# Kernel optimization log

Hardware: AMD Instinct MI355X
Metric: run time of the kernel (lower is better)

Reference implementation:

```python
import jax, jax.numpy as jnp
import numpy as np

B, T, D, S, K = 4, 4096, 1024, 2048, 4
LN_EPS = 1e-5


def setup_inputs() -> dict:
    key = jax.random.key(0)
    ks = jax.random.split(key, 9)
    scale = 0.02
    return {
        "x": jax.random.normal(ks[0], (B, T, D), jnp.float32),
        "W_in": jax.random.normal(ks[1], (D, 2 * S), jnp.float32) * scale,
        "b_in": jnp.zeros((2 * S,), jnp.float32),
        "conv_w": jax.random.normal(ks[2], (S, 1, K), jnp.float32) * scale,  # depthwise [out_ch, in_ch/groups=1, K]
        "conv_b": jnp.zeros((S,), jnp.float32),
        "W_out": jax.random.normal(ks[3], (S, D), jnp.float32) * scale,
        "b_out": jnp.zeros((D,), jnp.float32),
        "gamma": jnp.ones((D,), jnp.float32),
        "beta": jnp.zeros((D,), jnp.float32),
    }


def reference(x, W_in, b_in, conv_w, conv_b, W_out, b_out, gamma, beta):
    # x: [B, T, D]
    residual = x
    proj = x @ W_in + b_in                      # [B, T, 2S]
    mixed, gate = jnp.split(proj, 2, axis=-1)   # each [B, T, S]
    mixed = mixed * jax.nn.sigmoid(gate)
    h = jnp.transpose(mixed, (0, 2, 1))         # [B, S, T]
    k = conv_w.shape[-1]
    # torch pads both sides by K-1 then slices [:T] -> equivalent to causal left-pad K-1
    y = jax.lax.conv_general_dilated(
        h, conv_w,
        window_strides=(1,),
        padding=[(k - 1, 0)],
        dimension_numbers=("NCH", "OIH", "NCH"),
        feature_group_count=conv_w.shape[0],
    ) + conv_b[None, :, None]                   # [B, S, T]
    y = jnp.transpose(y, (0, 2, 1))             # [B, T, S]
    y = y @ W_out + b_out                       # [B, T, D]
    z = residual + y                            # dropout p=0.0 -> identity
    mu = jnp.mean(z, axis=-1, keepdims=True)
    var = jnp.var(z, axis=-1, keepdims=True)
    zn = (z - mu) * jax.lax.rsqrt(var + LN_EPS)
    return zn * gamma + beta
```

## Files before the change

### kernel.cpp

```cpp
#include <hip/hip_runtime.h>
#include <hip/hip_bf16.h>


#define Bdim 4
#define Tdim 4096
#define Ddim 1024
#define Sdim 2048
#define Mdim (Bdim * Tdim)
#define LN_EPS 1e-5f

typedef __bf16 bf16;
typedef __bf16 bf16x8 __attribute__((ext_vector_type(8)));
typedef float f32x4 __attribute__((ext_vector_type(4)));

#define BAR() __builtin_amdgcn_s_barrier()
#define SCHED() __builtin_amdgcn_sched_barrier(0)
#define LGKM0() asm volatile("s_waitcnt lgkmcnt(0)" ::: "memory")
#define VMCNT4() asm volatile("s_waitcnt vmcnt(4)" ::: "memory")
#define VMCNT0() asm volatile("s_waitcnt vmcnt(0)" ::: "memory")

__device__ __forceinline__ void gload_lds16(const bf16* g, bf16* l) {
  __builtin_amdgcn_global_load_lds((const __attribute__((address_space(1))) void*)g,
                                   (__attribute__((address_space(3))) void*)l,
                                   16, 0, 0);
}

__device__ __forceinline__ f32x4 zero4() {
  f32x4 z; z[0] = 0.f; z[1] = 0.f; z[2] = 0.f; z[3] = 0.f; return z;
}

__global__ __launch_bounds__(256) void k_cast_x(const float* __restrict__ x,
                                                bf16* __restrict__ xb) {
  int gid = blockIdx.x * 256 + threadIdx.x;
  const float4* p = (const float4*)x + (size_t)gid * 2;
  float4 a = p[0], b = p[1];
  bf16x8 o;
  o[0] = (bf16)a.x; o[1] = (bf16)a.y; o[2] = (bf16)a.z; o[3] = (bf16)a.w;
  o[4] = (bf16)b.x; o[5] = (bf16)b.y; o[6] = (bf16)b.z; o[7] = (bf16)b.w;
  ((bf16x8*)xb)[gid] = o;
}

__global__ __launch_bounds__(256) void k_transpose_cast(const float* __restrict__ in,
                                                        bf16* __restrict__ out,
                                                        int R, int C, int permmode) {
  __shared__ float tile[32][33];
  int tx = threadIdx.x & 31;
  int ty = threadIdx.x >> 5;
  int r0 = blockIdx.y * 32;
  int c0 = blockIdx.x * 32;
#pragma unroll
  for (int i = 0; i < 4; ++i)
    tile[ty + i * 8][tx] = in[(size_t)(r0 + ty + i * 8) * C + c0 + tx];
  __syncthreads();
#pragma unroll
  for (int i = 0; i < 4; ++i) {
    int oc = c0 + ty + i * 8;
    int pr = oc;
    if (permmode) {
      pr = (oc < 2048) ? ((oc >> 4) * 32 + (oc & 15))
                       : (((oc - 2048) >> 4) * 32 + 16 + (oc & 15));
    }
    out[(size_t)pr * R + r0 + tx] = (bf16)tile[tx][ty + i * 8];
  }
}

template<int KTOT, int NTN, int EPI>
__global__ __launch_bounds__(512, 1)
void k_gemm256(const bf16* __restrict__ Ag, const bf16* __restrict__ Bg,
               const float* __restrict__ bias, const float* __restrict__ xres,
               bf16* __restrict__ outb, float* __restrict__ outf) {
  __shared__ __attribute__((aligned(16))) char lds[131072];

  const int tid = threadIdx.x;
  const int w = tid >> 6, lane = tid & 63;
  const int lr = lane & 15, lk = lane >> 4;
  const int wr = w >> 2, wc = w & 3;

  const int nwg = gridDim.x;
  const int bid = blockIdx.x;
  const int wg = (bid & 7) * (nwg >> 3) + (bid >> 3);
  const int m0 = (wg / NTN) * 256;
  const int n0 = (wg % NTN) * 256;

  const int dlin = lane * 16;
  const int lsw = dlin ^ (((dlin >> 7) & 7) << 4);
  const int rw = lsw >> 7;
  const int cw = (lsw & 127) >> 1;

  const int xmask = (lr & 7) << 4;
  const int arow = lr * 128;
  const int brow = ((wc & 1) * 64 + lr) * 128;
  const char* ldsA = lds + wr * 16384;
  const char* ldsB = lds + 32768 + (wc >> 1) * 16384;

  auto stage = [&](const bf16* G, int row0, int kt, int regionByte) {
#pragma unroll
    for (int L = 0; L < 2; ++L) {
      int q = w * 2 + L;
      const bf16* src = G + (size_t)(row0 + q * 8 + rw) * KTOT + kt * 64 + cw;
      gload_lds16(src, (bf16*)(lds + regionByte + q * 1024));
    }
  };
  auto rdA = [&](int s, int mi, int ks) -> bf16x8 {
    return *(const bf16x8*)(ldsA + s * 65536 + mi * 2048 + arow +
                            ((ks * 64 + lk * 16) ^ xmask));
  };
  auto rdB = [&](int s, int nj, int ks) -> bf16x8 {
    return *(const bf16x8*)(ldsB + s * 65536 + nj * 2048 + brow +
                            ((ks * 64 + lk * 16) ^ xmask));
  };

  f32x4 acc[8][4];
#pragma unroll
  for (int i = 0; i < 8; ++i)
#pragma unroll
    for (int j = 0; j < 4; ++j) acc[i][j] = zero4();

  bf16x8 a[4][2], b[4][2];

#define QUAD(rh, ch)                                                                   \
  {                                                                                    \
    _Pragma("unroll")                                                                  \
    for (int mi = 0; mi < 4; ++mi) {                                                   \
      _Pragma("unroll")                                                                \
      for (int nj = 0; nj < 2; ++nj) {                                                 \
        acc[(rh)*4+mi][(ch)*2+nj] = __builtin_amdgcn_mfma_f32_16x16x32_bf16(           \
            a[mi][0], b[(ch)*2+nj][0], acc[(rh)*4+mi][(ch)*2+nj], 0, 0, 0);            \
        acc[(rh)*4+mi][(ch)*2+nj] = __builtin_amdgcn_mfma_f32_16x16x32_bf16(           \
            a[mi][1], b[(ch)*2+nj][1], acc[(rh)*4+mi][(ch)*2+nj], 0, 0, 0);            \
      }                                                                                \
    }                                                                                  \
  }

  const int NI = KTOT / 128;

  stage(Bg, n0,       0, 32768);
  stage(Bg, n0 + 128, 0, 32768 + 16384);
  stage(Ag, m0,       0, 0);
  stage(Ag, m0 + 128, 0, 16384);
  stage(Bg, n0,       1, 65536 + 32768);
  stage(Bg, n0 + 128, 1, 65536 + 32768 + 16384);
  VMCNT4(); BAR();

  for (int i = 0; i < NI; ++i) {
    const int kta2 = 2 * i + 2;
    const int ktb  = 2 * i + 1;
    const bool nl = (i < NI - 1);

#pragma unroll
    for (int mi = 0; mi < 4; ++mi) { a[mi][0] = rdA(0, mi, 0); a[mi][1] = rdA(0, mi, 1); }
#pragma unroll
    for (int nj = 0; nj < 2; ++nj) { b[nj][0] = rdB(0, nj, 0); b[nj][1] = rdB(0, nj, 1); }
    stage(Ag, m0, ktb, 65536);
    asm volatile("s_waitcnt lgkmcnt(8)" ::: "memory");
    BAR(); LGKM0(); SCHED();
    __builtin_amdgcn_s_setprio(1); QUAD(0, 0); __builtin_amdgcn_s_setprio(0);
    BAR();

#pragma unroll
    for (int nj = 0; nj < 2; ++nj) { b[2+nj][0] = rdB(0, 2+nj, 0); b[2+nj][1] = rdB(0, 2+nj, 1); }
    stage(Ag, m0 + 128, ktb, 65536 + 16384);
    BAR(); LGKM0(); SCHED();
    __builtin_amdgcn_s_setprio(1); QUAD(0, 1); __builtin_amdgcn_s_setprio(0);
    BAR();

#pragma unroll
    for (int mi = 0; mi < 4; ++mi) { a[mi][0] = rdA(0, 4+mi, 0); a[mi][1] = rdA(0, 4+mi, 1); }
    if (nl) stage(Bg, n0, kta2, 32768);
    BAR(); LGKM0(); SCHED();
    __builtin_amdgcn_s_setprio(1); QUAD(1, 0); __builtin_amdgcn_s_setprio(0);
    BAR();

    if (nl) stage(Bg, n0 + 128, kta2, 32768 + 16384);
    BAR(); LGKM0(); SCHED();
    __builtin_amdgcn_s_setprio(1); QUAD(1, 1); __builtin_amdgcn_s_setprio(0);
    if (nl) { VMCNT4(); } else { VMCNT0(); }
    BAR();

#pragma unroll
    for (int mi = 0; mi < 4; ++mi) { a[mi][0] = rdA(1, mi, 0); a[mi][1] = rdA(1, mi, 1); }
#pragma unroll
    for (int nj = 0; nj < 2; ++nj) { b[nj][0] = rdB(1, nj, 0); b[nj][1] = rdB(1, nj, 1); }
    if (nl) stage(Ag, m0, kta2, 0);
    asm volatile("s_waitcnt lgkmcnt(8)" ::: "memory");
    BAR(); LGKM0(); SCHED();
    __builtin_amdgcn_s_setprio(1); QUAD(0, 0); __builtin_amdgcn_s_setprio(0);
    BAR();

#pragma unroll
    for (int nj = 0; nj < 2; ++nj) { b[2+nj][0] = rdB(1, 2+nj, 0); b[2+nj][1] = rdB(1, 2+nj, 1); }
    if (nl) stage(Ag, m0 + 128, kta2, 16384);
    BAR(); LGKM0(); SCHED();
    __builtin_amdgcn_s_setprio(1); QUAD(0, 1); __builtin_amdgcn_s_setprio(0);
    BAR();

#pragma unroll
    for (int mi = 0; mi < 4; ++mi) { a[mi][0] = rdA(1, 4+mi, 0); a[mi][1] = rdA(1, 4+mi, 1); }
    if (nl) stage(Bg, n0, ktb + 2, 65536 + 32768);
    BAR(); LGKM0(); SCHED();
    __builtin_amdgcn_s_setprio(1); QUAD(1, 0); __builtin_amdgcn_s_setprio(0);
    BAR();

    if (nl) stage(Bg, n0 + 128, ktb + 2, 65536 + 32768 + 16384);
    BAR(); LGKM0(); SCHED();
    __builtin_amdgcn_s_setprio(1); QUAD(1, 1); __builtin_amdgcn_s_setprio(0);
    if (nl) { VMCNT4(); }
    BAR();
  }
#undef QUAD

  if (EPI == 0) {
#pragma unroll
    for (int p = 0; p < 2; ++p) {
      const int g = (n0 + wc * 64 + p * 32) >> 5;
      const int mcol = g * 16 + lr;
      const float bm = bias[mcol];
      const float bg = bias[mcol + 2048];
#pragma unroll
      for (int mi = 0; mi < 8; ++mi)
#pragma unroll
        for (int ii = 0; ii < 4; ++ii) {
          const int row = m0 + wr * 128 + mi * 16 + lk * 4 + ii;
          const float pm = acc[mi][2 * p][ii] + bm;
          const float pg = acc[mi][2 * p + 1][ii] + bg;
          outb[(size_t)row * Sdim + mcol] = (bf16)(pm / (1.0f + __expf(-pg)));
        }
    }
  } else {
#pragma unroll
    for (int nj = 0; nj < 4; ++nj) {
      const int col = n0 + wc * 64 + nj * 16 + lr;
      const float bo = bias[col];
#pragma unroll
      for (int mi = 0; mi < 8; ++mi)
#pragma unroll
        for (int ii = 0; ii < 4; ++ii) {
          const int row = m0 + wr * 128 + mi * 16 + lk * 4 + ii;
          const size_t idx = (size_t)row * Ddim + col;
          outf[idx] = xres[idx] + bo + acc[mi][nj][ii];
        }
    }
  }
}

__global__ __launch_bounds__(256) void k_conv(const bf16* __restrict__ mixed,
                                              const float* __restrict__ cw,
                                              const float* __restrict__ cb,
                                              bf16* __restrict__ h) {
  int gid = blockIdx.x * 256 + threadIdx.x;
  int cg = gid & 255;
  int tg = (gid >> 8) & 511;
  int bb = gid >> 17;
  int ch0 = cg * 8;
  int t0 = tg * 8;
  const size_t base = ((size_t)bb * Tdim) * Sdim + ch0;

  float4 w4[8];
  float bias[8];
#pragma unroll
  for (int j = 0; j < 8; ++j) {
    w4[j] = ((const float4*)cw)[ch0 + j];
    bias[j] = cb[ch0 + j];
  }

  bf16x8 zv;
#pragma unroll
  for (int j = 0; j < 8; ++j) zv[j] = (bf16)0.0f;

  bf16x8 win[11];
#pragma unroll
  for (int i = 0; i < 11; ++i) {
    int t = t0 - 3 + i;
    win[i] = (t >= 0) ? *(const bf16x8*)(mixed + base + (size_t)t * Sdim) : zv;
  }

#pragma unroll
  for (int i = 0; i < 8; ++i) {
    bf16x8 o;
#pragma unroll
    for (int j = 0; j < 8; ++j) {
      float aa = bias[j]
              + w4[j].x * (float)win[i + 0][j]
              + w4[j].y * (float)win[i + 1][j]
              + w4[j].z * (float)win[i + 2][j]
              + w4[j].w * (float)win[i + 3][j];
      o[j] = (bf16)aa;
    }
    *(bf16x8*)(h + base + (size_t)(t0 + i) * Sdim) = o;
  }
}

__global__ __launch_bounds__(256) void k_ln(const float* __restrict__ z,
                                            const float* __restrict__ gamma,
                                            const float* __restrict__ beta,
                                            float* __restrict__ out) {
  int row = blockIdx.x;
  int tid = threadIdx.x;
  const float4* zr = (const float4*)(z + (size_t)row * Ddim);
  float4 v = zr[tid];
  float s = v.x + v.y + v.z + v.w;
  float ss = v.x * v.x + v.y * v.y + v.z * v.z + v.w * v.w;
#pragma unroll
  for (int off = 32; off > 0; off >>= 1) {
    s += __shfl_xor(s, off);
    ss += __shfl_xor(ss, off);
  }
  __shared__ float ps[4], pss[4];
  int wave = tid >> 6, lane = tid & 63;
  if (lane == 0) { ps[wave] = s; pss[wave] = ss; }
  __syncthreads();
  float tots = ps[0] + ps[1] + ps[2] + ps[3];
  float totss = pss[0] + pss[1] + pss[2] + pss[3];
  float mu = tots * (1.0f / (float)Ddim);
  float var = totss * (1.0f / (float)Ddim) - mu * mu;
  float rs = rsqrtf(var + LN_EPS);
  float4 gg = ((const float4*)gamma)[tid];
  float4 bb = ((const float4*)beta)[tid];
  float4 o;
  o.x = (v.x - mu) * rs * gg.x + bb.x;
  o.y = (v.y - mu) * rs * gg.y + bb.y;
  o.z = (v.z - mu) * rs * gg.z + bb.z;
  o.w = (v.w - mu) * rs * gg.w + bb.w;
  ((float4*)(out + (size_t)row * Ddim))[tid] = o;
}

extern "C" void kernel_launch(void* const* d_in, const int* in_sizes, int n_in,
                              void* d_out, int out_size, void* d_ws, size_t ws_size,
                              hipStream_t stream) {
  const float* x = (const float*)d_in[0];
  const float* W_in = (const float*)d_in[1];
  const float* b_in = (const float*)d_in[2];
  const float* conv_w = (const float*)d_in[3];
  const float* conv_b = (const float*)d_in[4];
  const float* W_out = (const float*)d_in[5];
  const float* b_out = (const float*)d_in[6];
  const float* gamma = (const float*)d_in[7];
  const float* beta = (const float*)d_in[8];
  float* out = (float*)d_out;

  char* ws = (char*)d_ws;
  bf16* mixed = (bf16*)ws;
  bf16* hbuf = (bf16*)(ws + ((size_t)64 << 20));
  bf16* xb = (bf16*)(ws + ((size_t)128 << 20));
  bf16* winT = (bf16*)(ws + ((size_t)160 << 20));
  bf16* woutT = (bf16*)(ws + ((size_t)168 << 20));
  float* z = (float*)mixed;

  k_cast_x<<<dim3(Mdim * Ddim / 8 / 256), dim3(256), 0, stream>>>(x, xb);
  k_transpose_cast<<<dim3(4096 / 32, 1024 / 32), dim3(256), 0, stream>>>(W_in, winT, 1024, 4096, 1);
  k_transpose_cast<<<dim3(1024 / 32, 2048 / 32), dim3(256), 0, stream>>>(W_out, woutT, 2048, 1024, 0);

  k_gemm256<1024, 16, 0><<<dim3(Mdim / 256 * (4096 / 256)), dim3(512), 0, stream>>>(
      xb, winT, b_in, nullptr, mixed, nullptr);

  k_conv<<<dim3(Bdim * (Tdim / 8) * (Sdim / 8) / 256), dim3(256), 0, stream>>>(
      mixed, conv_w, conv_b, hbuf);

  k_gemm256<2048, 4, 1><<<dim3(Mdim / 256 * (Ddim / 256)), dim3(512), 0, stream>>>(
      hbuf, woutT, b_out, x, nullptr, z);

  k_ln<<<dim3(Mdim), dim3(256), 0, stream>>>(z, gamma, beta, out);
}
```

Baseline: 450.2 us.

## Double-buffer A fragments in GEMM to overlap LDS reads with MFMA

Splits the A-fragment registers into two sets so the next half-tile's A operands are read from LDS while the current quadrant's MFMAs run, and prefetches the next k-step's A before the loop iteration ends. Wait counts are relaxed (lgkmcnt(8), vmcnt(2)) to allow more outstanding loads. Launch bounds are changed to request 2 workgroups per CU, which tightens the register budget. The 128KB static LDS allocation is unchanged, so that second workgroup may not fit, and the tighter register budget risks spills with the extra fragment registers. The reworked waitcnt and barrier placement also risks hazards.

New measurement: 699.0 us. +55.3%, slower.

```diff
diff --git a/kernel.cpp b/kernel.cpp
--- a/kernel.cpp
+++ b/kernel.cpp
@@ -16,7 +16,9 @@
 #define BAR() __builtin_amdgcn_s_barrier()
 #define SCHED() __builtin_amdgcn_sched_barrier(0)
 #define LGKM0() asm volatile("s_waitcnt lgkmcnt(0)" ::: "memory")
+#define LGKM8() asm volatile("s_waitcnt lgkmcnt(8)" ::: "memory")
 #define VMCNT4() asm volatile("s_waitcnt vmcnt(4)" ::: "memory")
+#define VMCNT2() asm volatile("s_waitcnt vmcnt(2)" ::: "memory")
 #define VMCNT0() asm volatile("s_waitcnt vmcnt(0)" ::: "memory")
 
 __device__ __forceinline__ void gload_lds16(const bf16* g, bf16* l) {
@@ -65,7 +67,7 @@
 }
 
 template<int KTOT, int NTN, int EPI>
-__global__ __launch_bounds__(512, 1)
+__global__ __launch_bounds__(512, 2)
 void k_gemm256(const bf16* __restrict__ Ag, const bf16* __restrict__ Bg,
                const float* __restrict__ bias, const float* __restrict__ xres,
                bf16* __restrict__ outb, float* __restrict__ outf) {
@@ -116,19 +118,35 @@
 #pragma unroll
     for (int j = 0; j < 4; ++j) acc[i][j] = zero4();
 
-  bf16x8 a[4][2], b[4][2];
-
-#define QUAD(rh, ch)                                                                   \
+  bf16x8 a1[4][2], a2[4][2], b[4][2];
+
+#define QUAD(A, rh, ch)                                                                \
   {                                                                                    \
     _Pragma("unroll")                                                                  \
     for (int mi = 0; mi < 4; ++mi) {                                                   \
       _Pragma("unroll")                                                                \
       for (int nj = 0; nj < 2; ++nj) {                                                 \
         acc[(rh)*4+mi][(ch)*2+nj] = __builtin_amdgcn_mfma_f32_16x16x32_bf16(           \
-            a[mi][0], b[(ch)*2+nj][0], acc[(rh)*4+mi][(ch)*2+nj], 0, 0, 0);            \
+            A[mi][0], b[(ch)*2+nj][0], acc[(rh)*4+mi][(ch)*2+nj], 0, 0, 0);            \
         acc[(rh)*4+mi][(ch)*2+nj] = __builtin_amdgcn_mfma_f32_16x16x32_bf16(           \
-            a[mi][1], b[(ch)*2+nj][1], acc[(rh)*4+mi][(ch)*2+nj], 0, 0, 0);            \
+            A[mi][1], b[(ch)*2+nj][1], acc[(rh)*4+mi][(ch)*2+nj], 0, 0, 0);            \
       }                                                                                \
+    }                                                                                  \
+  }
+#define RD_A(DST, s, base)                                                             \
+  {                                                                                    \
+    _Pragma("unroll")                                                                  \
+    for (int mi = 0; mi < 4; ++mi) {                                                   \
+      DST[mi][0] = rdA(s, (base) + mi, 0);                                             \
+      DST[mi][1] = rdA(s, (base) + mi, 1);                                             \
+    }                                                                                  \
+  }
+#define RD_B(s, base)                                                                  \
+  {                                                                                    \
+    _Pragma("unroll")                                                                  \
+    for (int nj = 0; nj < 2; ++nj) {                                                   \
+      b[(base)+nj][0] = rdB(s, (base) + nj, 0);                                        \
+      b[(base)+nj][1] = rdB(s, (base) + nj, 1);                                        \
     }                                                                                  \
   }
 
@@ -140,74 +158,67 @@
   stage(Ag, m0 + 128, 0, 16384);
   stage(Bg, n0,       1, 65536 + 32768);
   stage(Bg, n0 + 128, 1, 65536 + 32768 + 16384);
-  VMCNT4(); BAR();
+  VMCNT4(); BAR(); SCHED();
+  RD_A(a1, 0, 0);
 
   for (int i = 0; i < NI; ++i) {
     const int kta2 = 2 * i + 2;
     const int ktb  = 2 * i + 1;
     const bool nl = (i < NI - 1);
 
-#pragma unroll
-    for (int mi = 0; mi < 4; ++mi) { a[mi][0] = rdA(0, mi, 0); a[mi][1] = rdA(0, mi, 1); }
-#pragma unroll
-    for (int nj = 0; nj < 2; ++nj) { b[nj][0] = rdB(0, nj, 0); b[nj][1] = rdB(0, nj, 1); }
+    RD_B(0, 0);
     stage(Ag, m0, ktb, 65536);
-    asm volatile("s_waitcnt lgkmcnt(8)" ::: "memory");
     BAR(); LGKM0(); SCHED();
-    __builtin_amdgcn_s_setprio(1); QUAD(0, 0); __builtin_amdgcn_s_setprio(0);
-    BAR();
-
-#pragma unroll
-    for (int nj = 0; nj < 2; ++nj) { b[2+nj][0] = rdB(0, 2+nj, 0); b[2+nj][1] = rdB(0, 2+nj, 1); }
+    __builtin_amdgcn_s_setprio(1); QUAD(a1, 0, 0); __builtin_amdgcn_s_setprio(0);
+    BAR();
+
+    RD_B(0, 2);
+    RD_A(a2, 0, 4);
     stage(Ag, m0 + 128, ktb, 65536 + 16384);
-    BAR(); LGKM0(); SCHED();
-    __builtin_amdgcn_s_setprio(1); QUAD(0, 1); __builtin_amdgcn_s_setprio(0);
-    BAR();
-
-#pragma unroll
-    for (int mi = 0; mi < 4; ++mi) { a[mi][0] = rdA(0, 4+mi, 0); a[mi][1] = rdA(0, 4+mi, 1); }
+    BAR(); LGKM8(); SCHED();
+    __builtin_amdgcn_s_setprio(1); QUAD(a1, 0, 1); __builtin_amdgcn_s_setprio(0);
+    BAR();
+
     if (nl) stage(Bg, n0, kta2, 32768);
     BAR(); LGKM0(); SCHED();
-    __builtin_amdgcn_s_setprio(1); QUAD(1, 0); __builtin_amdgcn_s_setprio(0);
-    BAR();
-
+    __builtin_amdgcn_s_setprio(1); QUAD(a2, 1, 0); __builtin_amdgcn_s_setprio(0);
+    if (nl) { VMCNT2(); } else { VMCNT0(); }
+    BAR(); SCHED();
+
+    RD_A(a1, 1, 0);
     if (nl) stage(Bg, n0 + 128, kta2, 32768 + 16384);
+    BAR();
+    __builtin_amdgcn_s_setprio(1); QUAD(a2, 1, 1); __builtin_amdgcn_s_setprio(0);
+    BAR();
+
+    RD_B(1, 0);
+    if (nl) stage(Ag, m0, kta2, 0);
     BAR(); LGKM0(); SCHED();
-    __builtin_amdgcn_s_setprio(1); QUAD(1, 1); __builtin_amdgcn_s_setprio(0);
-    if (nl) { VMCNT4(); } else { VMCNT0(); }
-    BAR();
-
-#pragma unroll
-    for (int mi = 0; mi < 4; ++mi) { a[mi][0] = rdA(1, mi, 0); a[mi][1] = rdA(1, mi, 1); }
-#pragma unroll
-    for (int nj = 0; nj < 2; ++nj) { b[nj][0] = rdB(1, nj, 0); b[nj][1] = rdB(1, nj, 1); }
-    if (nl) stage(Ag, m0, kta2, 0);
-    asm volatile("s_waitcnt lgkmcnt(8)" ::: "memory");
-    BAR(); LGKM0(); SCHED();
-    __builtin_amdgcn_s_setprio(1); QUAD(0, 0); __builtin_amdgcn_s_setprio(0);
-    BAR();
-
-#pragma unroll
-    for (int nj = 0; nj < 2; ++nj) { b[2+nj][0] = rdB(1, 2+nj, 0); b[2+nj][1] = rdB(1, 2+nj, 1); }
+    __builtin_amdgcn_s_setprio(1); QUAD(a1, 0, 0); __builtin_amdgcn_s_setprio(0);
+    BAR();
+
+    RD_B(1, 2);
+    RD_A(a2, 1, 4);
     if (nl) stage(Ag, m0 + 128, kta2, 16384);
-    BAR(); LGKM0(); SCHED();
-    __builtin_amdgcn_s_setprio(1); QUAD(0, 1); __builtin_amdgcn_s_setprio(0);
-    BAR();
-
-#pragma unroll
-    for (int mi = 0; mi < 4; ++mi) { a[mi][0] = rdA(1, 4+mi, 0); a[mi][1] = rdA(1, 4+mi, 1); }
+    BAR(); LGKM8(); SCHED();
+    __builtin_amdgcn_s_setprio(1); QUAD(a1, 0, 1); __builtin_amdgcn_s_setprio(0);
+    BAR();
+
     if (nl) stage(Bg, n0, ktb + 2, 65536 + 32768);
     BAR(); LGKM0(); SCHED();
-    __builtin_amdgcn_s_setprio(1); QUAD(1, 0); __builtin_amdgcn_s_setprio(0);
-    BAR();
-
+    __builtin_amdgcn_s_setprio(1); QUAD(a2, 1, 0); __builtin_amdgcn_s_setprio(0);
+    if (nl) { VMCNT2(); }
+    BAR(); SCHED();
+
+    if (nl) { RD_A(a1, 0, 0); }
     if (nl) stage(Bg, n0 + 128, ktb + 2, 65536 + 32768 + 16384);
-    BAR(); LGKM0(); SCHED();
-    __builtin_amdgcn_s_setprio(1); QUAD(1, 1); __builtin_amdgcn_s_setprio(0);
-    if (nl) { VMCNT4(); }
+    BAR();
+    __builtin_amdgcn_s_setprio(1); QUAD(a2, 1, 1); __builtin_amdgcn_s_setprio(0);
     BAR();
   }
 #undef QUAD
+#undef RD_A
+#undef RD_B
 
   if (EPI == 0) {
 #pragma unroll
```
